# Kernel optimization log

Measured on AMD Instinct MI355X. Metric: run time of the kernel, lower is better.

Reference implementation:

```python
import jax, jax.numpy as jnp
import numpy as np
from jax import lax

LOW_T = 25.0    # int(0.1 * 255)
HIGH_T = 76.0   # int(0.3 * 255)
HYST_ITERS = 64 # cap on hysteresis propagation sweeps
TG22 = 0.4142135623730951  # tan(22.5 deg)
TG67 = 2.414213562373095   # tan(67.5 deg)

SOBEL_X = jnp.array([[-1., 0., 1.], [-2., 0., 2.], [-1., 0., 1.]], dtype=jnp.float32)
SOBEL_Y = jnp.array([[-1., -2., -1.], [0., 0., 0.], [1., 2., 1.]], dtype=jnp.float32)


def _conv3(x, k):
    # x: [B,H,W]; reflect-101 border like cv2.Sobel default
    xp = jnp.pad(x, ((0, 0), (1, 1), (1, 1)), mode='reflect')
    return lax.conv_general_dilated(xp[:, None], k[None, None], (1, 1), 'VALID')[:, 0]


def _dilate3x3(m):
    # 3x3 max-pool (8-connected dilation); m is nonnegative float 0/1
    return lax.reduce_window(m, jnp.float32(0.0), lax.max, (1, 3, 3), (1, 1, 1), 'SAME')


def canny_edge(image, low, high):
    """Batched Canny. image: [B,C,H,W] in [0,1] -> edges [B,1,H,W] in {0,1}."""
    image = lax.stop_gradient(image)  # mirrors .cpu().detach().numpy()
    B, C, H, W = image.shape
    if C == 3:
        gray = 0.299 * image[:, 0] + 0.587 * image[:, 1] + 0.114 * image[:, 2]
    else:
        gray = image[:, 0]
    # (img*255).astype(np.uint8) == floor toward zero for values in [0,1]
    g = jnp.clip(jnp.floor(gray * 255.0), 0.0, 255.0)

    gx = _conv3(g, SOBEL_X)
    gy = _conv3(g, SOBEL_Y)
    mag = jnp.abs(gx) + jnp.abs(gy)  # cv2 default L2gradient=False -> L1 magnitude

    # --- non-maximum suppression (OpenCV-style direction quantization) ---
    mp = jnp.pad(mag, ((0, 0), (1, 1), (1, 1)))

    def sh(dy, dx):
        return mp[:, 1 + dy:1 + dy + H, 1 + dx:1 + dx + W]

    ax, ay = jnp.abs(gx), jnp.abs(gy)
    horiz = ay <= TG22 * ax              # gradient ~horizontal: compare L/R
    vert = ay >= TG67 * ax               # gradient ~vertical: compare U/D
    diag = ~(horiz | vert)
    same_sign = (gx * gy) >= 0
    d1 = diag & same_sign                # 45 deg diagonal

    keep_h = (mag > sh(0, -1)) & (mag >= sh(0, 1))
    keep_v = (mag > sh(-1, 0)) & (mag >= sh(1, 0))
    keep_d1 = (mag > sh(-1, -1)) & (mag >= sh(1, 1))
    keep_d2 = (mag > sh(-1, 1)) & (mag >= sh(1, -1))
    keep = jnp.where(horiz, keep_h,
           jnp.where(vert, keep_v,
           jnp.where(d1, keep_d1, keep_d2)))
    nms = jnp.where(keep, mag, 0.0)

    # --- double threshold + hysteresis (iterative 8-connected propagation) ---
    weak = (nms > low).astype(jnp.float32)
    strong = (nms > high).astype(jnp.float32)

    def cond(state):
        cur, prev, i = state
        return jnp.logical_and(i < HYST_ITERS, jnp.any(cur != prev))

    def body(state):
        cur, prev, i = state
        new = jnp.minimum(_dilate3x3(cur), weak)          # grow strong into weak
        new = jnp.maximum(new, strong)
        return new, cur, i + 1

    edges, _, _ = lax.while_loop(cond, body, (strong, -jnp.ones_like(strong), 0))
    return edges[:, None]  # [B,1,H,W]


def reference(image_A, image_B):
    image_A = jnp.where(image_A.max() > 1, image_A / 2.0, image_A)
    image_B = jnp.where(image_B.max() > 1, image_B / 2.0, image_B)
    edges_A = canny_edge(image_A, LOW_T, HIGH_T)
    edges_B = canny_edge(image_B, LOW_T, HIGH_T)
    diff = edges_A - edges_B
    return jnp.sqrt(jnp.sum(diff * diff))  # Frobenius norm over all elements


def setup_inputs() -> dict:
    key = jax.random.key(0)
    kA, kB = jax.random.split(key)
    image_A = jax.random.uniform(kA, (32, 3, 512, 512), dtype=jnp.float32)
    image_B = jax.random.uniform(kB, (32, 3, 512, 512), dtype=jnp.float32)
    return {"image_A": image_A, "image_B": image_B}
```

## Files before the change

kernel.cpp:

```cpp
#include <hip/hip_runtime.h>
#include <cstdint>

typedef unsigned long long u64;
typedef unsigned int u32;
typedef unsigned char u8;

__device__ __forceinline__ int reflect_row(int t) {
    return t < 0 ? -t : (t > 511 ? 1022 - t : t);
}

__device__ __forceinline__ float gray255(float r, float g, float b) {
    return fminf(fmaxf(floorf((0.299f * r + 0.587f * g + 0.114f * b) * 255.0f), 0.0f), 255.0f);
}

__global__ __launch_bounds__(256) void gray_kernel(
    const float* __restrict__ imgA, const float* __restrict__ imgB,
    u32* __restrict__ gray4, u32* __restrict__ counters)
{
    if (threadIdx.x == 0 && blockIdx.x == 0 && blockIdx.z == 0) {
        counters[0] = 0u;
        counters[1] = 0u;
    }
    const int img = blockIdx.z;
    const float* src = (img < 32) ? imgA + (size_t)img * 786432
                                  : imgB + (size_t)(img - 32) * 786432;
    const int i4 = blockIdx.x * 256 + threadIdx.x;
    float4 r = ((const float4*)(src          ))[i4];
    float4 g = ((const float4*)(src + 262144))[i4];
    float4 b = ((const float4*)(src + 524288))[i4];
    u32 p0 = (u32)gray255(r.x, g.x, b.x);
    u32 p1 = (u32)gray255(r.y, g.y, b.y);
    u32 p2 = (u32)gray255(r.z, g.z, b.z);
    u32 p3 = (u32)gray255(r.w, g.w, b.w);
    gray4[(size_t)img * 65536 + i4] = p0 | (p1 << 8) | (p2 << 16) | (p3 << 24);
}

__global__ __launch_bounds__(256, 4) void canny8(
    const u8* __restrict__ gray,
    u8* __restrict__ strong_b, u8* __restrict__ weak_b)
{
    const int lane = threadIdx.x & 63;
    const int wid  = threadIdx.x >> 6;
    const int band = blockIdx.x * 4 + wid;
    const int img  = blockIdx.y;
    const int y0   = band * 8;
    const u8* src  = gray + (size_t)img * 262144 + lane * 8;
    const bool lane0 = (lane == 0), lane63 = (lane == 63);

    float s[3][8], d[3][8], m[3][8];
    float lm[3], rm[3];
    u32 clsA = 0, clsB = 0;

    uint2 pr = *(const uint2*)(src + (size_t)reflect_row(y0 - 2) * 512);

    #pragma unroll
    for (int i = 0; i < 12; ++i) {
        const int t = y0 - 2 + i;
        const uint2 cur = pr;
        pr = *(const uint2*)(src + (size_t)reflect_row(t + 1) * 512);

        float g[8];
        #pragma unroll
        for (int k = 0; k < 4; ++k) {
            g[k]     = (float)((cur.x >> (8 * k)) & 0xffu);
            g[4 + k] = (float)((cur.y >> (8 * k)) & 0xffu);
        }
        float gl = __shfl_up(g[7], 1);
        float gr = __shfl_down(g[0], 1);
        if (lane0)  gl = g[1];
        if (lane63) gr = g[6];

        const int k2 = i % 3;
        #pragma unroll
        for (int j = 0; j < 8; ++j) {
            const float a = (j == 0) ? gl : g[j - 1];
            const float c = (j == 7) ? gr : g[j + 1];
            s[k2][j] = a + 2.f * g[j] + c;
            d[k2][j] = c - a;
        }

        if (i >= 2) {
            const int k0 = (i - 2) % 3, k1 = (i - 1) % 3;
            const bool rowok = ((unsigned)(t - 1) < 512u);
            u32 cls = 0;
            #pragma unroll
            for (int j = 0; j < 8; ++j) {
                const float gx = d[k0][j] + 2.f * d[k1][j] + d[k2][j];
                const float gy = s[k2][j] - s[k0][j];
                const float ax = fabsf(gx), ay = fabsf(gy);
                m[k2][j] = rowok ? (ax + ay) : 0.f;
                const bool horiz = ay <= 0.4142135623730951f * ax;
                const bool vert  = ay >= 2.414213562373095f * ax;
                const bool ss    = gx * gy >= 0.0f;
                const u32 code = horiz ? 0u : (vert ? 1u : (ss ? 2u : 3u));
                cls |= code << (2 * j);
            }
            const float lmn = __shfl_up(m[k2][7], 1);
            const float rmn = __shfl_down(m[k2][0], 1);
            lm[k2] = lane0  ? 0.f : lmn;
            rm[k2] = lane63 ? 0.f : rmn;
            clsA = clsB; clsB = cls;

            if (i >= 4) {
                const int up = (i - 2) % 3, ct = (i - 1) % 3, dn = k2;
                u32 nw = 0, ns = 0;
                #pragma unroll
                for (int j = 0; j < 8; ++j) {
                    const float C0 = m[up][j], C1 = m[ct][j], C2 = m[dn][j];
                    const float L0 = (j == 0) ? lm[up] : m[up][j - 1];
                    const float L1 = (j == 0) ? lm[ct] : m[ct][j - 1];
                    const float L2 = (j == 0) ? lm[dn] : m[dn][j - 1];
                    const float R0 = (j == 7) ? rm[up] : m[up][j + 1];
                    const float R1 = (j == 7) ? rm[ct] : m[ct][j + 1];
                    const float R2 = (j == 7) ? rm[dn] : m[dn][j + 1];
                    const u32 code = (clsA >> (2 * j)) & 3u;
                    const bool keep =
                        (code == 0u) ? (C1 > L1 && C1 >= R1) :
                        (code == 1u) ? (C1 > C0 && C1 >= C2) :
                        (code == 2u) ? (C1 > L0 && C1 >= R2)
                                     : (C1 > R0 && C1 >= L2);
                    nw |= (keep && C1 > 25.0f ? 1u : 0u) << j;
                    ns |= (keep && C1 > 76.0f ? 1u : 0u) << j;
                }
                const size_t o = ((size_t)img * 512 + (t - 2)) * 64 + lane;
                weak_b[o]   = (u8)nw;
                strong_b[o] = (u8)ns;
            }
        }
    }
}

__global__ __launch_bounds__(128) void hyst_diff_kernel(
    const u64* __restrict__ strong_in, const u64* __restrict__ weak_in,
    unsigned int* __restrict__ sum, unsigned int* __restrict__ done,
    float* __restrict__ out)
{
    const int pair = blockIdx.z;
    const int ty = blockIdx.y, tx = blockIdx.x;
    const int half = threadIdx.x >> 6;
    const int lane = threadIdx.x & 63;
    const int img = pair + (half ? 32 : 0);

    __shared__ u64 bint[128 * 2];

    const int row0 = ty * 128 - 64;
    const int wc0  = tx * 2 - 1;
    const size_t ibase = (size_t)img * 512 * 8;

    u64 c[4][4], wk[4][4];
    #pragma unroll
    for (int r = 0; r < 4; ++r) {
        int gr = row0 + lane * 4 + r;
        bool rok = (gr >= 0 && gr < 512);
        #pragma unroll
        for (int j = 0; j < 4; ++j) {
            int wc = wc0 + j;
            bool ok = rok && wc >= 0 && wc < 8;
            size_t o = ibase + (size_t)gr * 8 + wc;
            c[r][j]  = ok ? strong_in[o] : 0ULL;
            wk[r][j] = ok ? weak_in[o]   : 0ULL;
        }
    }

    for (int it = 0; it < 64; ++it) {
        u64 h[4][4];
        #pragma unroll
        for (int r = 0; r < 4; ++r) {
            h[r][0] = c[r][0] | (c[r][0] << 1) | (c[r][0] >> 1) | (c[r][1] << 63);
            h[r][1] = c[r][1] | (c[r][1] << 1) | (c[r][1] >> 1) | (c[r][0] >> 63) | (c[r][2] << 63);
            h[r][2] = c[r][2] | (c[r][2] << 1) | (c[r][2] >> 1) | (c[r][1] >> 63) | (c[r][3] << 63);
            h[r][3] = c[r][3] | (c[r][3] << 1) | (c[r][3] >> 1) | (c[r][2] >> 63);
        }
        u64 delta = 0ULL;
        #pragma unroll
        for (int j = 0; j < 4; ++j) {
            u64 top = __shfl_up(h[3][j], 1);
            u64 bot = __shfl_down(h[0][j], 1);
            if (lane == 0)  top = 0ULL;
            if (lane == 63) bot = 0ULL;
            u64 n0 = (h[0][j] | top     | h[1][j]) & wk[0][j];
            u64 n1 = (h[1][j] | h[0][j] | h[2][j]) & wk[1][j];
            u64 n2 = (h[2][j] | h[1][j] | h[3][j]) & wk[2][j];
            u64 n3 = (h[3][j] | h[2][j] | bot    ) & wk[3][j];
            delta |= (n0 ^ c[0][j]) | (n1 ^ c[1][j]) | (n2 ^ c[2][j]) | (n3 ^ c[3][j]);
            c[0][j] = n0; c[1][j] = n1; c[2][j] = n2; c[3][j] = n3;
        }
        if (__ballot(delta != 0ULL) == 0ULL) break;
    }

    if (half == 1 && lane >= 16 && lane < 48) {
        #pragma unroll
        for (int r = 0; r < 4; ++r) {
            int lr = lane * 4 + r - 64;
            bint[lr * 2 + 0] = c[r][1];
            bint[lr * 2 + 1] = c[r][2];
        }
    }
    __syncthreads();

    unsigned int v = 0;
    if (half == 0 && lane >= 16 && lane < 48) {
        #pragma unroll
        for (int r = 0; r < 4; ++r) {
            int lr = lane * 4 + r - 64;
            v += (unsigned int)__popcll(c[r][1] ^ bint[lr * 2 + 0]);
            v += (unsigned int)__popcll(c[r][2] ^ bint[lr * 2 + 1]);
        }
    }
    #pragma unroll
    for (int off = 32; off > 0; off >>= 1) v += __shfl_down(v, off);

    if (threadIdx.x == 0) {
        if (v != 0) atomicAdd(sum, v);
        __threadfence();
        unsigned int ticket = atomicAdd(done, 1);
        if (ticket == 4 * 4 * 32 - 1) {
            __threadfence();
            unsigned int s = atomicAdd(sum, 0u);
            out[0] = sqrtf((float)s);
        }
    }
}

extern "C" void kernel_launch(void* const* d_in, const int* in_sizes, int n_in,
                              void* d_out, int out_size, void* d_ws, size_t ws_size,
                              hipStream_t stream) {
    const float* imgA = (const float*)d_in[0];
    const float* imgB = (const float*)d_in[1];
    float* out = (float*)d_out;
    char* ws = (char*)d_ws;
    u64* strong_m = (u64*)(ws);
    u64* weak_m   = (u64*)(ws + (2u << 20));
    unsigned int* counters = (unsigned int*)(ws + (4u << 20));
    u32* gray4    = (u32*)(ws + (5u << 20));

    dim3 g0(256, 1, 64);
    gray_kernel<<<g0, 256, 0, stream>>>(imgA, imgB, gray4, counters);

    dim3 g1(16, 64);
    canny8<<<g1, 256, 0, stream>>>((const u8*)gray4, (u8*)strong_m, (u8*)weak_m);

    dim3 g2(4, 4, 32);
    hyst_diff_kernel<<<g2, 128, 0, stream>>>(strong_m, weak_m,
                                             counters, counters + 1, out);
}
```

Baseline: 252.8 us.

## Fuse grayscale conversion into Canny kernel reading RGB floats directly

The separate grayscale kernel is removed and the Canny band kernel now loads the three float RGB planes directly, computing the quantized gray values in registers. Band height grows from 8 to 16 rows so the two halo rows are a smaller fraction of each band, and the grid halves to match. This drops the gray buffer write and re-read plus one kernel launch. In exchange, halo rows are reloaded as full float RGB at 12 bytes per pixel rather than 1, each thread holds more registers for its prefetched row, and there are fewer blocks.

After: 325.4 us. 1.29x slower.

```diff
diff --git a/kernel.cpp b/kernel.cpp
--- a/kernel.cpp
+++ b/kernel.cpp
@@ -13,58 +13,65 @@
     return fminf(fmaxf(floorf((0.299f * r + 0.587f * g + 0.114f * b) * 255.0f), 0.0f), 255.0f);
 }
 
-__global__ __launch_bounds__(256) void gray_kernel(
+__global__ __launch_bounds__(256, 3) void canny_rgb(
     const float* __restrict__ imgA, const float* __restrict__ imgB,
-    u32* __restrict__ gray4, u32* __restrict__ counters)
+    u8* __restrict__ strong_b, u8* __restrict__ weak_b,
+    u32* __restrict__ counters)
 {
-    if (threadIdx.x == 0 && blockIdx.x == 0 && blockIdx.z == 0) {
+    if (threadIdx.x == 0 && blockIdx.x == 0 && blockIdx.y == 0) {
         counters[0] = 0u;
         counters[1] = 0u;
     }
-    const int img = blockIdx.z;
-    const float* src = (img < 32) ? imgA + (size_t)img * 786432
-                                  : imgB + (size_t)(img - 32) * 786432;
-    const int i4 = blockIdx.x * 256 + threadIdx.x;
-    float4 r = ((const float4*)(src          ))[i4];
-    float4 g = ((const float4*)(src + 262144))[i4];
-    float4 b = ((const float4*)(src + 524288))[i4];
-    u32 p0 = (u32)gray255(r.x, g.x, b.x);
-    u32 p1 = (u32)gray255(r.y, g.y, b.y);
-    u32 p2 = (u32)gray255(r.z, g.z, b.z);
-    u32 p3 = (u32)gray255(r.w, g.w, b.w);
-    gray4[(size_t)img * 65536 + i4] = p0 | (p1 << 8) | (p2 << 16) | (p3 << 24);
-}
-
-__global__ __launch_bounds__(256, 4) void canny8(
-    const u8* __restrict__ gray,
-    u8* __restrict__ strong_b, u8* __restrict__ weak_b)
-{
     const int lane = threadIdx.x & 63;
     const int wid  = threadIdx.x >> 6;
     const int band = blockIdx.x * 4 + wid;
     const int img  = blockIdx.y;
-    const int y0   = band * 8;
-    const u8* src  = gray + (size_t)img * 262144 + lane * 8;
+    const int y0   = band * 16;
+    const float* src = ((img < 32) ? imgA + (size_t)img * 786432
+                                   : imgB + (size_t)(img - 32) * 786432)
+                       + lane * 8;
     const bool lane0 = (lane == 0), lane63 = (lane == 63);
 
     float s[3][8], d[3][8], m[3][8];
     float lm[3], rm[3];
     u32 clsA = 0, clsB = 0;
 
-    uint2 pr = *(const uint2*)(src + (size_t)reflect_row(y0 - 2) * 512);
+    float4 nR0, nR1, nG0, nG1, nB0, nB1;
+    {
+        const float* p = src + (size_t)reflect_row(y0 - 2) * 512;
+        nR0 = *(const float4*)(p);
+        nR1 = *(const float4*)(p + 4);
+        nG0 = *(const float4*)(p + 262144);
+        nG1 = *(const float4*)(p + 262148);
+        nB0 = *(const float4*)(p + 524288);
+        nB1 = *(const float4*)(p + 524292);
+    }
 
     #pragma unroll
-    for (int i = 0; i < 12; ++i) {
+    for (int i = 0; i < 20; ++i) {
         const int t = y0 - 2 + i;
-        const uint2 cur = pr;
-        pr = *(const uint2*)(src + (size_t)reflect_row(t + 1) * 512);
+        const float4 cR0 = nR0, cR1 = nR1, cG0 = nG0, cG1 = nG1,
+                     cB0 = nB0, cB1 = nB1;
+        {
+            const float* p = src + (size_t)reflect_row(t + 1) * 512;
+            nR0 = *(const float4*)(p);
+            nR1 = *(const float4*)(p + 4);
+            nG0 = *(const float4*)(p + 262144);
+            nG1 = *(const float4*)(p + 262148);
+            nB0 = *(const float4*)(p + 524288);
+            nB1 = *(const float4*)(p + 524292);
+        }
 
         float g[8];
-        #pragma unroll
-        for (int k = 0; k < 4; ++k) {
-            g[k]     = (float)((cur.x >> (8 * k)) & 0xffu);
-            g[4 + k] = (float)((cur.y >> (8 * k)) & 0xffu);
-        }
+        g[0] = gray255(cR0.x, cG0.x, cB0.x);
+        g[1] = gray255(cR0.y, cG0.y, cB0.y);
+        g[2] = gray255(cR0.z, cG0.z, cB0.z);
+        g[3] = gray255(cR0.w, cG0.w, cB0.w);
+        g[4] = gray255(cR1.x, cG1.x, cB1.x);
+        g[5] = gray255(cR1.y, cG1.y, cB1.y);
+        g[6] = gray255(cR1.z, cG1.z, cB1.z);
+        g[7] = gray255(cR1.w, cG1.w, cB1.w);
+
         float gl = __shfl_up(g[7], 1);
         float gr = __shfl_down(g[0], 1);
         if (lane0)  gl = g[1];
@@ -232,13 +239,10 @@
     u64* strong_m = (u64*)(ws);
     u64* weak_m   = (u64*)(ws + (2u << 20));
     unsigned int* counters = (unsigned int*)(ws + (4u << 20));
-    u32* gray4    = (u32*)(ws + (5u << 20));
-
-    dim3 g0(256, 1, 64);
-    gray_kernel<<<g0, 256, 0, stream>>>(imgA, imgB, gray4, counters);
-
-    dim3 g1(16, 64);
-    canny8<<<g1, 256, 0, stream>>>((const u8*)gray4, (u8*)strong_m, (u8*)weak_m);
+
+    dim3 g1(8, 64);
+    canny_rgb<<<g1, 256, 0, stream>>>(imgA, imgB,
+                                      (u8*)strong_m, (u8*)weak_m, counters);
 
     dim3 g2(4, 4, 32);
     hyst_diff_kernel<<<g2, 128, 0, stream>>>(strong_m, weak_m,
```
